# Performance work log

Measured on AMD Instinct MI355X. Metric: run time of the kernel, lower is better.

The kernel has to match this reference:

```python
import jax, jax.numpy as jnp
import numpy as np

B = 48        # graphs per batch
NODES = 330   # hardcoded in forward (x.view(batch_size, 330, hidden))
N = B * NODES # 15840 nodes
DEG = 16
E = N * DEG   # 253440 edges
IN_CH = 128
HID = 256
OUT_CH = 1
EDGE_DIM = 5
EPS = 1e-5


def _lin(key, out_f, in_f):
    k1, k2 = jax.random.split(key)
    s = 1.0 / np.sqrt(in_f)
    W = jax.random.uniform(k1, (out_f, in_f), minval=-s, maxval=s, dtype=jnp.float32)
    b = jax.random.uniform(k2, (out_f,), minval=-s, maxval=s, dtype=jnp.float32)
    return W, b


def setup_inputs() -> dict:
    key = jax.random.key(0)
    ks = jax.random.split(key, 10)
    x = jax.random.normal(ks[0], (N, IN_CH), dtype=jnp.float32)
    edge_index = jax.random.randint(ks[1], (2, E), 0, N, dtype=jnp.int32)
    edge_attr = jax.random.normal(ks[2], (E, EDGE_DIM), dtype=jnp.float32)
    batch = (jnp.arange(N, dtype=jnp.int32) // NODES)
    Wq, bq = _lin(ks[3], HID, IN_CH)
    Wk, bk = _lin(ks[4], HID, IN_CH)
    Wv, bv = _lin(ks[5], HID, IN_CH)
    se = 1.0 / np.sqrt(EDGE_DIM)
    We = jax.random.uniform(ks[6], (HID, EDGE_DIM), minval=-se, maxval=se, dtype=jnp.float32)  # lin_edge, bias=False
    Wskip, bskip = _lin(ks[7], HID, IN_CH)
    ln_g = jnp.ones((IN_CH,), jnp.float32); ln_b = jnp.zeros((IN_CH,), jnp.float32)
    bn_g = jnp.ones((HID,), jnp.float32); bn_b = jnp.zeros((HID,), jnp.float32)
    W1, b1 = _lin(ks[8], HID, HID)
    Wr, br = _lin(ks[9], OUT_CH, HID)
    return dict(x=x, edge_index=edge_index, edge_attr=edge_attr, batch=batch,
                Wq=Wq, bq=bq, Wk=Wk, bk=bk, Wv=Wv, bv=bv, We=We,
                Wskip=Wskip, bskip=bskip, ln_g=ln_g, ln_b=ln_b,
                bn_g=bn_g, bn_b=bn_b, W1=W1, b1=b1, Wr=Wr, br=br)


def _forward(x, edge_index, edge_attr, batch,
             Wq, bq, Wk, bk, Wv, bv, We, Wskip, bskip,
             ln_g, ln_b, bn_g, bn_b, W1, b1, Wr, br):
    n = x.shape[0]
    bs = batch.shape[0] // NODES
    # self.norm -> assumed LayerNorm over features
    mu = x.mean(-1, keepdims=True)
    var = x.var(-1, keepdims=True)
    x = (x - mu) / jnp.sqrt(var + EPS) * ln_g + ln_b

    # TransformerConv (heads=1, edge_dim=5, root_weight=True)
    src, dst = edge_index[0], edge_index[1]
    q = x @ Wq.T + bq                      # [N, HID]
    k = x @ Wk.T + bk
    v = x @ Wv.T + bv
    e = edge_attr @ We.T                   # [E, HID]
    ke = k[src] + e                        # edge-conditioned keys
    ve = v[src] + e                        # edge-conditioned values
    alpha = (q[dst] * ke).sum(-1) / jnp.sqrt(jnp.float32(HID))  # [E]
    m = jax.ops.segment_max(alpha, dst, num_segments=n)
    a = jnp.exp(alpha - m[dst])
    z = jax.ops.segment_sum(a, dst, num_segments=n)
    a = a / (z[dst] + 1e-16)               # PyG softmax guard
    out = jax.ops.segment_sum(a[:, None] * ve, dst, num_segments=n)
    out = out + x @ Wskip.T + bskip        # root/skip connection

    # BatchNorm1d (training-mode batch stats) + relu
    bm = out.mean(0)
    bv_ = out.var(0)
    out = (out - bm) / jnp.sqrt(bv_ + EPS) * bn_g + bn_b
    out = jax.nn.relu(out)

    # pooling chain over the node axis: 330 -> 110 -> 36 -> 18
    h = out.reshape(bs, NODES, HID).transpose(0, 2, 1)   # [B, HID, 330]
    h = h.reshape(bs, HID, 110, 3).max(-1)               # k3 s3
    h = h[:, :, :108].reshape(bs, HID, 36, 3).max(-1)    # k3 s3 (floor)
    h = h.reshape(bs, HID, 18, 2).max(-1)                # k2 s2
    h = h.transpose(0, 2, 1)                             # [B, 18, HID]

    h = jax.nn.relu(h @ W1.T + b1)
    c = (h @ Wr.T + br).mean(axis=1)                     # [B, OUT]
    return jax.nn.sigmoid(c).squeeze(-1)                 # [B]


def reference(x, edge_index, edge_attr, batch, Wq, bq, Wk, bk, Wv, bv, We,
              Wskip, bskip, ln_g, ln_b, bn_g, bn_b, W1, b1, Wr, br):
    return _forward(x, edge_index, edge_attr, batch, Wq, bq, Wk, bk, Wv, bv,
                    We, Wskip, bskip, ln_g, ln_b, bn_g, bn_b, W1, b1, Wr, br)
```

## Files before the change

kernel.cpp:

```cpp
#include <hip/hip_runtime.h>
#include <math.h>

#define NNODES 15840
#define NEDGES 253440
#define INCH 128
#define HIDC 256
#define BGR 48
#define GNODES 330
#define SLOT 56

typedef __attribute__((ext_vector_type(8))) short bf16x8;
typedef __attribute__((ext_vector_type(4))) float f32x4;
typedef __attribute__((ext_vector_type(2))) float f32x2;

__device__ inline unsigned short f2bf(float f) {
  union { float f; unsigned int u; } v; v.f = f;
  unsigned int u = v.u;
  u += 0x7fff + ((u >> 16) & 1);
  return (unsigned short)(u >> 16);
}
__device__ inline float bf2f(unsigned short h) {
  union { unsigned int u; float f; } v; v.u = ((unsigned int)h) << 16;
  return v.f;
}
__device__ inline unsigned char f2fp8(float f) {
  int p = __builtin_amdgcn_cvt_pk_fp8_f32(f, f, 0, false);
  return (unsigned char)(p & 0xff);
}

#define LN_BLOCKS 3960
#define WC_BLOCKS 128
#define BUILD_BLOCKS 990
__global__ __launch_bounds__(256) void prep_kernel(
    const float* __restrict__ x, const float* __restrict__ g, const float* __restrict__ b,
    unsigned short* __restrict__ Xhi, unsigned short* __restrict__ Xlo,
    const float* __restrict__ Wq, const float* __restrict__ bq,
    const float* __restrict__ Wk, const float* __restrict__ bk,
    const float* __restrict__ Wv, const float* __restrict__ bv,
    const float* __restrict__ Ws, const float* __restrict__ bs,
    unsigned short* __restrict__ Whi, unsigned short* __restrict__ Wlo,
    float* __restrict__ bbig,
    const int* __restrict__ src, const int* __restrict__ dst,
    const float* __restrict__ ea, int* __restrict__ cursor,
    int* __restrict__ src_perm, float* __restrict__ ea_perm) {
  int blk = blockIdx.x, t = threadIdx.x;
  if (blk < LN_BLOCKS) {
    int wid = blk * 4 + (t >> 6);
    int lane = t & 63;
    float2 v = *(const float2*)(x + (size_t)wid * INCH + lane * 2);
    float s = v.x + v.y;
#pragma unroll
    for (int o = 32; o > 0; o >>= 1) s += __shfl_xor(s, o);
    float mean = s * (1.0f / INCH);
    float d0 = v.x - mean, d1 = v.y - mean;
    float sq = d0 * d0 + d1 * d1;
#pragma unroll
    for (int o = 32; o > 0; o >>= 1) sq += __shfl_xor(sq, o);
    float rstd = rsqrtf(sq * (1.0f / INCH) + 1e-5f);
    float2 gg = *(const float2*)(g + lane * 2);
    float2 bb = *(const float2*)(b + lane * 2);
    float o0 = d0 * rstd * gg.x + bb.x;
    float o1 = d1 * rstd * gg.y + bb.y;
    unsigned short h0 = f2bf(o0), h1 = f2bf(o1);
    unsigned short l0 = f2bf(o0 - bf2f(h0)), l1 = f2bf(o1 - bf2f(h1));
    ushort2 hh; hh.x = h0; hh.y = h1;
    ushort2 ll; ll.x = l0; ll.y = l1;
    *(ushort2*)(Xhi + (size_t)wid * INCH + lane * 2) = hh;
    *(ushort2*)(Xlo + (size_t)wid * INCH + lane * 2) = ll;
  } else if (blk < LN_BLOCKS + WC_BLOCKS) {
    int idx = (blk - LN_BLOCKS) * 256 + t;
    int n = idx >> 5;
    int k0 = (idx & 31) * 4;
    const float* W;
    switch (n >> 8) {
      case 0:  W = Wq; break;
      case 1:  W = Wk; break;
      case 2:  W = Wv; break;
      default: W = Ws; break;
    }
    int r = n & 255;
    float4 w4 = *(const float4*)(W + (size_t)r * 128 + k0);
    ushort4 hi, lo;
    hi.x = f2bf(w4.x); lo.x = f2bf(w4.x - bf2f(hi.x));
    hi.y = f2bf(w4.y); lo.y = f2bf(w4.y - bf2f(hi.y));
    hi.z = f2bf(w4.z); lo.z = f2bf(w4.z - bf2f(hi.z));
    hi.w = f2bf(w4.w); lo.w = f2bf(w4.w - bf2f(hi.w));
    *(ushort4*)(Whi + (size_t)n * 128 + k0) = hi;
    *(ushort4*)(Wlo + (size_t)n * 128 + k0) = lo;
    if (idx < 1024) {
      const float* bsrc;
      switch (idx >> 8) {
        case 0:  bsrc = bq; break;
        case 1:  bsrc = bk; break;
        case 2:  bsrc = bv; break;
        default: bsrc = bs; break;
      }
      bbig[idx] = bsrc[idx & 255];
    }
  } else {
    int e = (blk - LN_BLOCKS - WC_BLOCKS) * 256 + t;
    if (e < NEDGES) {
      int d = dst[e];
      int pos = atomicAdd(&cursor[d], 1);
      if (pos < SLOT) {
        int slot = d * SLOT + pos;
        src_perm[slot] = src[e];
        const float* ap = ea + (size_t)e * 5;
        float* op = ea_perm + (size_t)slot * 5;
#pragma unroll
        for (int i = 0; i < 5; i++) op[i] = ap[i];
      }
    }
  }
}

__global__ __launch_bounds__(256, 2) void gemm_mfma(
    const unsigned short* __restrict__ Xhi, const unsigned short* __restrict__ Xlo,
    const unsigned short* __restrict__ Whi, const unsigned short* __restrict__ Wlo,
    const float* __restrict__ bbig,
    float* __restrict__ QS, unsigned char* __restrict__ KV8) {
  int lane = threadIdx.x & 63;
  int w = threadIdx.x >> 6;
  int m0 = blockIdx.x * 64;
  int quad = lane >> 4;
  int lr = lane & 15;

  const bf16x8 zf = {0, 0, 0, 0, 0, 0, 0, 0};
  bf16x8 A[4][2][4];
#pragma unroll
  for (int tI = 0; tI < 4; tI++) {
    int row = m0 + tI * 16 + lr;
    bool ok = row < NNODES;
    const unsigned short* ph = Xhi + (size_t)row * 128 + quad * 8;
    const unsigned short* pl = Xlo + (size_t)row * 128 + quad * 8;
#pragma unroll
    for (int kf = 0; kf < 4; kf++) {
      A[tI][0][kf] = ok ? *(const bf16x8*)(ph + kf * 32) : zf;
      A[tI][1][kf] = ok ? *(const bf16x8*)(pl + kf * 32) : zf;
    }
  }

  int ntbase = (blockIdx.y * 4 + w) * 8;
#pragma unroll 2
  for (int i = 0; i < 8; i++) {
    int n0 = (ntbase + i) * 16;
    const unsigned short* wh = Whi + (size_t)(n0 + lr) * 128 + quad * 8;
    const unsigned short* wl = Wlo + (size_t)(n0 + lr) * 128 + quad * 8;
    bf16x8 Bh[4], Bl[4];
#pragma unroll
    for (int kf = 0; kf < 4; kf++) {
      Bh[kf] = *(const bf16x8*)(wh + kf * 32);
      Bl[kf] = *(const bf16x8*)(wl + kf * 32);
    }
    f32x4 acc[4];
#pragma unroll
    for (int m = 0; m < 4; m++) acc[m] = (f32x4){0.f, 0.f, 0.f, 0.f};
#pragma unroll
    for (int kf = 0; kf < 4; kf++) {
#pragma unroll
      for (int m = 0; m < 4; m++)
        acc[m] = __builtin_amdgcn_mfma_f32_16x16x32_bf16(A[m][0][kf], Bh[kf], acc[m], 0, 0, 0);
#pragma unroll
      for (int m = 0; m < 4; m++)
        acc[m] = __builtin_amdgcn_mfma_f32_16x16x32_bf16(A[m][0][kf], Bl[kf], acc[m], 0, 0, 0);
#pragma unroll
      for (int m = 0; m < 4; m++)
        acc[m] = __builtin_amdgcn_mfma_f32_16x16x32_bf16(A[m][1][kf], Bh[kf], acc[m], 0, 0, 0);
    }
    int col = n0 + lr;
    float bias = bbig[col];
    int mat = col >> 8;
    int cc = col & 255;
    int base_off = (mat == 0 || mat == 1) ? cc : 256 + cc;
    bool isF32 = (mat == 0 || mat == 3);
#pragma unroll
    for (int m = 0; m < 4; m++) {
#pragma unroll
      for (int r = 0; r < 4; r++) {
        int row = m0 + m * 16 + quad * 4 + r;
        if (row < NNODES) {
          float val = acc[m][r] + bias;
          if (isF32) QS[(size_t)row * 512 + base_off] = val;
          else       KV8[(size_t)row * 512 + base_off] = f2fp8(val);
        }
      }
    }
  }
}

__global__ __launch_bounds__(256) void agg_kernel(
    const float* __restrict__ QS, const unsigned char* __restrict__ KV8,
    const float* __restrict__ ea_perm, const float* __restrict__ We,
    const int* __restrict__ src_perm, const int* __restrict__ cursor,
    float* __restrict__ outb) {
  int t = threadIdx.x;
  int nd = blockIdx.x * 4 + (t >> 6);
  int lane = t & 63;
  if (nd >= NNODES) return;

  float4 q = *(const float4*)(QS + (size_t)nd * 512 + 4 * lane);

  float c5[5];
  {
    float wp0[5], wp1[5], wp2[5], wp3[5];
#pragma unroll
    for (int d = 0; d < 5; d++) {
      wp0[d] = We[(4 * lane + 0) * 5 + d];
      wp1[d] = We[(4 * lane + 1) * 5 + d];
      wp2[d] = We[(4 * lane + 2) * 5 + d];
      wp3[d] = We[(4 * lane + 3) * 5 + d];
    }
#pragma unroll
    for (int d = 0; d < 5; d++) {
      float s = q.x * wp0[d] + q.y * wp1[d] + q.z * wp2[d] + q.w * wp3[d];
#pragma unroll
      for (int o = 32; o > 0; o >>= 1) s += __shfl_xor(s, o);
      c5[d] = s;
    }
  }

  int deg = cursor[nd]; if (deg > SLOT) deg = SLOT;
  int beg = nd * SLOT, end = beg + deg;
  float m = -INFINITY, z = 0.0f;
  float ax = 0.f, ay = 0.f, az = 0.f, aw = 0.f;
  float ea_acc[5] = {0.f, 0.f, 0.f, 0.f, 0.f};

  int j = beg;
  for (; j + 4 <= end; j += 4) {
    int s0 = src_perm[j], s1 = src_perm[j + 1], s2 = src_perm[j + 2], s3 = src_perm[j + 3];
    const unsigned char* b0 = KV8 + (size_t)s0 * 512 + 4 * lane;
    const unsigned char* b1 = KV8 + (size_t)s1 * 512 + 4 * lane;
    const unsigned char* b2 = KV8 + (size_t)s2 * 512 + 4 * lane;
    const unsigned char* b3 = KV8 + (size_t)s3 * 512 + 4 * lane;
    unsigned int kw0 = *(const unsigned int*)b0;
    unsigned int kw1 = *(const unsigned int*)b1;
    unsigned int kw2 = *(const unsigned int*)b2;
    unsigned int kw3 = *(const unsigned int*)b3;
    unsigned int vw0 = *(const unsigned int*)(b0 + 256);
    unsigned int vw1 = *(const unsigned int*)(b1 + 256);
    unsigned int vw2 = *(const unsigned int*)(b2 + 256);
    unsigned int vw3 = *(const unsigned int*)(b3 + 256);
    float eat[4][5];
    {
      const float* ap = ea_perm + (size_t)j * 5;
#pragma unroll
      for (int i = 0; i < 4; i++)
#pragma unroll
        for (int d = 0; d < 5; d++) eat[i][d] = ap[i * 5 + d];
    }
    f32x2 ka0 = __builtin_amdgcn_cvt_pk_f32_fp8(kw0, false), kb0 = __builtin_amdgcn_cvt_pk_f32_fp8(kw0, true);
    f32x2 ka1 = __builtin_amdgcn_cvt_pk_f32_fp8(kw1, false), kb1 = __builtin_amdgcn_cvt_pk_f32_fp8(kw1, true);
    f32x2 ka2 = __builtin_amdgcn_cvt_pk_f32_fp8(kw2, false), kb2 = __builtin_amdgcn_cvt_pk_f32_fp8(kw2, true);
    f32x2 ka3 = __builtin_amdgcn_cvt_pk_f32_fp8(kw3, false), kb3 = __builtin_amdgcn_cvt_pk_f32_fp8(kw3, true);
    float p0 = q.x * ka0.x + q.y * ka0.y + q.z * kb0.x + q.w * kb0.y;
    float p1 = q.x * ka1.x + q.y * ka1.y + q.z * kb1.x + q.w * kb1.y;
    float p2 = q.x * ka2.x + q.y * ka2.y + q.z * kb2.x + q.w * kb2.y;
    float p3 = q.x * ka3.x + q.y * ka3.y + q.z * kb3.x + q.w * kb3.y;
#pragma unroll
    for (int o = 32; o > 0; o >>= 1) {
      p0 += __shfl_xor(p0, o); p1 += __shfl_xor(p1, o);
      p2 += __shfl_xor(p2, o); p3 += __shfl_xor(p3, o);
    }
    float dt0 = 0.f, dt1 = 0.f, dt2 = 0.f, dt3 = 0.f;
#pragma unroll
    for (int d = 0; d < 5; d++) {
      dt0 += c5[d] * eat[0][d]; dt1 += c5[d] * eat[1][d];
      dt2 += c5[d] * eat[2][d]; dt3 += c5[d] * eat[3][d];
    }
    float al0 = (p0 + dt0) * 0.0625f, al1 = (p1 + dt1) * 0.0625f;
    float al2 = (p2 + dt2) * 0.0625f, al3 = (p3 + dt3) * 0.0625f;
    float bm = fmaxf(fmaxf(al0, al1), fmaxf(al2, al3));
    float nm = fmaxf(m, bm);
    float sc = __expf(m - nm);
    float w0 = __expf(al0 - nm), w1 = __expf(al1 - nm);
    float w2 = __expf(al2 - nm), w3 = __expf(al3 - nm);
    f32x2 va0 = __builtin_amdgcn_cvt_pk_f32_fp8(vw0, false), vb0 = __builtin_amdgcn_cvt_pk_f32_fp8(vw0, true);
    f32x2 va1 = __builtin_amdgcn_cvt_pk_f32_fp8(vw1, false), vb1 = __builtin_amdgcn_cvt_pk_f32_fp8(vw1, true);
    f32x2 va2 = __builtin_amdgcn_cvt_pk_f32_fp8(vw2, false), vb2 = __builtin_amdgcn_cvt_pk_f32_fp8(vw2, true);
    f32x2 va3 = __builtin_amdgcn_cvt_pk_f32_fp8(vw3, false), vb3 = __builtin_amdgcn_cvt_pk_f32_fp8(vw3, true);
    z = z * sc + (w0 + w1 + w2 + w3);
    ax = ax * sc + w0 * va0.x + w1 * va1.x + w2 * va2.x + w3 * va3.x;
    ay = ay * sc + w0 * va0.y + w1 * va1.y + w2 * va2.y + w3 * va3.y;
    az = az * sc + w0 * vb0.x + w1 * vb1.x + w2 * vb2.x + w3 * vb3.x;
    aw = aw * sc + w0 * vb0.y + w1 * vb1.y + w2 * vb2.y + w3 * vb3.y;
#pragma unroll
    for (int d = 0; d < 5; d++)
      ea_acc[d] = ea_acc[d] * sc + w0 * eat[0][d] + w1 * eat[1][d] + w2 * eat[2][d] + w3 * eat[3][d];
    m = nm;
  }
  for (; j < end; j++) {
    int s = src_perm[j];
    const unsigned char* bp = KV8 + (size_t)s * 512 + 4 * lane;
    unsigned int kw = *(const unsigned int*)bp;
    unsigned int vw = *(const unsigned int*)(bp + 256);
    float eat[5];
    const float* ap = ea_perm + (size_t)j * 5;
#pragma unroll
    for (int d = 0; d < 5; d++) eat[d] = ap[d];
    f32x2 ka = __builtin_amdgcn_cvt_pk_f32_fp8(kw, false), kb = __builtin_amdgcn_cvt_pk_f32_fp8(kw, true);
    float p = q.x * ka.x + q.y * ka.y + q.z * kb.x + q.w * kb.y;
#pragma unroll
    for (int o = 32; o > 0; o >>= 1) p += __shfl_xor(p, o);
    float dt = 0.f;
#pragma unroll
    for (int d = 0; d < 5; d++) dt += c5[d] * eat[d];
    float al = (p + dt) * 0.0625f;
    float nm = fmaxf(m, al);
    float sc = __expf(m - nm);
    float wgt = __expf(al - nm);
    f32x2 va = __builtin_amdgcn_cvt_pk_f32_fp8(vw, false), vb = __builtin_amdgcn_cvt_pk_f32_fp8(vw, true);
    z = z * sc + wgt;
    ax = ax * sc + wgt * va.x; ay = ay * sc + wgt * va.y;
    az = az * sc + wgt * vb.x; aw = aw * sc + wgt * vb.y;
#pragma unroll
    for (int d = 0; d < 5; d++) ea_acc[d] = ea_acc[d] * sc + wgt * eat[d];
    m = nm;
  }

  float inv = 1.0f / (z + 1e-16f);
  float4 sk = *(const float4*)(QS + (size_t)nd * 512 + 256 + 4 * lane);
  float efx = 0.f, efy = 0.f, efz = 0.f, efw = 0.f;
#pragma unroll
  for (int d = 0; d < 5; d++) {
    float ead = ea_acc[d];
    efx += We[(4 * lane + 0) * 5 + d] * ead;
    efy += We[(4 * lane + 1) * 5 + d] * ead;
    efz += We[(4 * lane + 2) * 5 + d] * ead;
    efw += We[(4 * lane + 3) * 5 + d] * ead;
  }
  float4 o;
  o.x = (ax + efx) * inv + sk.x;
  o.y = (ay + efy) * inv + sk.y;
  o.z = (az + efz) * inv + sk.z;
  o.w = (aw + efw) * inv + sk.w;
  *(float4*)(outb + (size_t)nd * HIDC + 4 * lane) = o;
}

__global__ void bnstat_kernel(const float* __restrict__ outb, float* __restrict__ sums,
                              float* __restrict__ sumsq) {
  int f = threadIdx.x;
  int r0 = blockIdx.x * 30;
  float s = 0.0f, sq = 0.0f;
  for (int r = 0; r < 30; r++) {
    float v = outb[(size_t)(r0 + r) * HIDC + f];
    s += v; sq += v * v;
  }
  atomicAdd(&sums[f], s);
  atomicAdd(&sumsq[f], sq);
}

__global__ __launch_bounds__(256) void pool_mlp_kernel(
    const float* __restrict__ outb, const float* __restrict__ sums,
    const float* __restrict__ sumsq, const float* __restrict__ bng,
    const float* __restrict__ bnb, const float* __restrict__ W1,
    const float* __restrict__ b1, const float* __restrict__ Wr,
    float* __restrict__ c) {
  __shared__ float hs[HIDC];
  __shared__ float red[HIDC];
  int bt = blockIdx.x, t = threadIdx.x;
  int b = bt / 18, tt = bt % 18;
  float mean = sums[t] * (1.0f / NNODES);
  float var = sumsq[t] * (1.0f / NNODES) - mean * mean;
  float scale = bng[t] * rsqrtf(var + 1e-5f);
  float shift = bnb[t] - mean * scale;
  int base = b * GNODES + tt * 18;
  float mx = -INFINITY;
  for (int r = 0; r < 18; r++) {
    float v = outb[(size_t)(base + r) * HIDC + t];
    mx = fmaxf(mx, fmaxf(v * scale + shift, 0.0f));
  }
  hs[t] = mx;
  __syncthreads();
  const float4* hv = (const float4*)hs;
  const float4* w = (const float4*)(W1 + t * HIDC);
  float acc = b1[t];
#pragma unroll 8
  for (int i = 0; i < HIDC / 4; i++) {
    float4 xi = hv[i]; float4 ww = w[i];
    acc += xi.x * ww.x + xi.y * ww.y + xi.z * ww.z + xi.w * ww.w;
  }
  red[t] = fmaxf(acc, 0.0f) * Wr[t];
  __syncthreads();
#pragma unroll
  for (int s = 128; s > 0; s >>= 1) {
    if (t < s) red[t] += red[t + s];
    __syncthreads();
  }
  if (t == 0) atomicAdd(&c[b], red[0] * (1.0f / 18.0f));
}

__global__ void final_kernel(const float* __restrict__ c, const float* __restrict__ br,
                             float* __restrict__ out) {
  int b = threadIdx.x;
  if (b < BGR) out[b] = 1.0f / (1.0f + expf(-(c[b] + br[0])));
}

extern "C" void kernel_launch(void* const* d_in, const int* in_sizes, int n_in,
                              void* d_out, int out_size, void* d_ws, size_t ws_size,
                              hipStream_t stream) {
  const float* x   = (const float*)d_in[0];
  const int*   ei  = (const int*)d_in[1];
  const float* ea  = (const float*)d_in[2];
  const float* Wq  = (const float*)d_in[4];  const float* bq  = (const float*)d_in[5];
  const float* Wk  = (const float*)d_in[6];  const float* bk  = (const float*)d_in[7];
  const float* Wv  = (const float*)d_in[8];  const float* bv  = (const float*)d_in[9];
  const float* We  = (const float*)d_in[10];
  const float* Wsk = (const float*)d_in[11]; const float* bsk = (const float*)d_in[12];
  const float* lng = (const float*)d_in[13]; const float* lnb = (const float*)d_in[14];
  const float* bng = (const float*)d_in[15]; const float* bnb = (const float*)d_in[16];
  const float* W1  = (const float*)d_in[17]; const float* b1  = (const float*)d_in[18];
  const float* Wr  = (const float*)d_in[19]; const float* br  = (const float*)d_in[20];
  float* outp = (float*)d_out;

  const int* srcArr = ei;
  const int* dstArr = ei + NEDGES;

  char* ws = (char*)d_ws;
  size_t off = 0;
  auto alloc = [&](size_t bytes) -> void* {
    void* p = ws + off;
    off += (bytes + 255) & ~(size_t)255;
    return p;
  };
  unsigned short* Xhi      = (unsigned short*)alloc((size_t)NNODES * INCH * 2);
  unsigned short* Xlo      = (unsigned short*)alloc((size_t)NNODES * INCH * 2);
  unsigned short* Whi      = (unsigned short*)alloc((size_t)1024 * 128 * 2);
  unsigned short* Wlo      = (unsigned short*)alloc((size_t)1024 * 128 * 2);
  float*          bbig     = (float*)alloc(1024 * 4);
  float*          QS       = (float*)alloc((size_t)NNODES * 512 * 4);
  unsigned char*  KV8      = (unsigned char*)alloc((size_t)NNODES * 512);
  float*          outb     = (float*)alloc((size_t)NNODES * HIDC * 4);
  int*            src_perm = (int*)alloc((size_t)NNODES * SLOT * 4);
  float*          ea_perm  = (float*)alloc((size_t)NNODES * SLOT * 5 * 4);
  size_t zn = (size_t)NNODES + HIDC * 2 + BGR;
  int* zblock = (int*)alloc(zn * 4);
  int*   cursor = zblock;
  float* sums   = (float*)(zblock + NNODES);
  float* sumsq  = sums + HIDC;
  float* cacc   = sumsq + HIDC;

  hipMemsetAsync(zblock, 0, zn * 4, stream);

  prep_kernel<<<LN_BLOCKS + WC_BLOCKS + BUILD_BLOCKS, 256, 0, stream>>>(
      x, lng, lnb, Xhi, Xlo, Wq, bq, Wk, bk, Wv, bv, Wsk, bsk, Whi, Wlo, bbig,
      srcArr, dstArr, ea, cursor, src_perm, ea_perm);
  gemm_mfma<<<dim3(248, 2), 256, 0, stream>>>(Xhi, Xlo, Whi, Wlo, bbig, QS, KV8);
  agg_kernel<<<NNODES / 4, 256, 0, stream>>>(QS, KV8, ea_perm, We, src_perm, cursor, outb);
  bnstat_kernel<<<528, 256, 0, stream>>>(outb, sums, sumsq);
  pool_mlp_kernel<<<BGR * 18, 256, 0, stream>>>(outb, sums, sumsq, bng, bnb, W1, b1, Wr, cacc);
  final_kernel<<<1, 64, 0, stream>>>(cacc, br, outp);
}
```

Measured before the change: 253.5 us.

## Pack edge src and attributes into 32-byte records and unroll aggregation by 8

The separate src_perm and ea_perm arrays are merged into one 8-float record per edge slot (source index bit-cast plus 5 attributes, padded), written with two float4 stores. The aggregation loop now processes 8 edges per iteration with two vector loads per edge and one clamped, masked tail in place of a separate scalar remainder loop. This is meant to cut load instruction count and raise memory-level parallelism for the gathered K/V reads. In exchange the padded layout moves more bytes, and masked tail lanes do redundant gathers for nodes whose degree is not a multiple of 8.

After: 282.9 us. 11.6% more time.

```diff
diff --git a/kernel.cpp b/kernel.cpp
--- a/kernel.cpp
+++ b/kernel.cpp
@@ -42,7 +42,7 @@
     float* __restrict__ bbig,
     const int* __restrict__ src, const int* __restrict__ dst,
     const float* __restrict__ ea, int* __restrict__ cursor,
-    int* __restrict__ src_perm, float* __restrict__ ea_perm) {
+    float* __restrict__ pack) {
   int blk = blockIdx.x, t = threadIdx.x;
   if (blk < LN_BLOCKS) {
     int wid = blk * 4 + (t >> 6);
@@ -103,12 +103,14 @@
       int d = dst[e];
       int pos = atomicAdd(&cursor[d], 1);
       if (pos < SLOT) {
-        int slot = d * SLOT + pos;
-        src_perm[slot] = src[e];
+        float* op = pack + ((size_t)d * SLOT + pos) * 8;
         const float* ap = ea + (size_t)e * 5;
-        float* op = ea_perm + (size_t)slot * 5;
-#pragma unroll
-        for (int i = 0; i < 5; i++) op[i] = ap[i];
+        float4 r0, r1;
+        r0.x = __int_as_float(src[e]);
+        r0.y = ap[0]; r0.z = ap[1]; r0.w = ap[2];
+        r1.x = ap[3]; r1.y = ap[4]; r1.z = 0.f; r1.w = 0.f;
+        *(float4*)op = r0;
+        *(float4*)(op + 4) = r1;
       }
     }
   }
@@ -190,9 +192,8 @@
 
 __global__ __launch_bounds__(256) void agg_kernel(
     const float* __restrict__ QS, const unsigned char* __restrict__ KV8,
-    const float* __restrict__ ea_perm, const float* __restrict__ We,
-    const int* __restrict__ src_perm, const int* __restrict__ cursor,
-    float* __restrict__ outb) {
+    const float* __restrict__ pack, const float* __restrict__ We,
+    const int* __restrict__ cursor, float* __restrict__ outb) {
   int t = threadIdx.x;
   int nd = blockIdx.x * 4 + (t >> 6);
   int lane = t & 63;
@@ -225,95 +226,68 @@
   float ax = 0.f, ay = 0.f, az = 0.f, aw = 0.f;
   float ea_acc[5] = {0.f, 0.f, 0.f, 0.f, 0.f};
 
-  int j = beg;
-  for (; j + 4 <= end; j += 4) {
-    int s0 = src_perm[j], s1 = src_perm[j + 1], s2 = src_perm[j + 2], s3 = src_perm[j + 3];
-    const unsigned char* b0 = KV8 + (size_t)s0 * 512 + 4 * lane;
-    const unsigned char* b1 = KV8 + (size_t)s1 * 512 + 4 * lane;
-    const unsigned char* b2 = KV8 + (size_t)s2 * 512 + 4 * lane;
-    const unsigned char* b3 = KV8 + (size_t)s3 * 512 + 4 * lane;
-    unsigned int kw0 = *(const unsigned int*)b0;
-    unsigned int kw1 = *(const unsigned int*)b1;
-    unsigned int kw2 = *(const unsigned int*)b2;
-    unsigned int kw3 = *(const unsigned int*)b3;
-    unsigned int vw0 = *(const unsigned int*)(b0 + 256);
-    unsigned int vw1 = *(const unsigned int*)(b1 + 256);
-    unsigned int vw2 = *(const unsigned int*)(b2 + 256);
-    unsigned int vw3 = *(const unsigned int*)(b3 + 256);
-    float eat[4][5];
-    {
-      const float* ap = ea_perm + (size_t)j * 5;
-#pragma unroll
-      for (int i = 0; i < 4; i++)
-#pragma unroll
-        for (int d = 0; d < 5; d++) eat[i][d] = ap[i * 5 + d];
-    }
-    f32x2 ka0 = __builtin_amdgcn_cvt_pk_f32_fp8(kw0, false), kb0 = __builtin_amdgcn_cvt_pk_f32_fp8(kw0, true);
-    f32x2 ka1 = __builtin_amdgcn_cvt_pk_f32_fp8(kw1, false), kb1 = __builtin_amdgcn_cvt_pk_f32_fp8(kw1, true);
-    f32x2 ka2 = __builtin_amdgcn_cvt_pk_f32_fp8(kw2, false), kb2 = __builtin_amdgcn_cvt_pk_f32_fp8(kw2, true);
-    f32x2 ka3 = __builtin_amdgcn_cvt_pk_f32_fp8(kw3, false), kb3 = __builtin_amdgcn_cvt_pk_f32_fp8(kw3, true);
-    float p0 = q.x * ka0.x + q.y * ka0.y + q.z * kb0.x + q.w * kb0.y;
-    float p1 = q.x * ka1.x + q.y * ka1.y + q.z * kb1.x + q.w * kb1.y;
-    float p2 = q.x * ka2.x + q.y * ka2.y + q.z * kb2.x + q.w * kb2.y;
-    float p3 = q.x * ka3.x + q.y * ka3.y + q.z * kb3.x + q.w * kb3.y;
+  for (int j0 = beg; j0 < end; j0 += 8) {
+    float4 pr0[8], pr1[8];
+#pragma unroll
+    for (int i = 0; i < 8; i++) {
+      int jj = j0 + i; jj = (jj < end) ? jj : (end - 1);
+      const float4* pp = (const float4*)(pack + (size_t)jj * 8);
+      pr0[i] = pp[0];
+      pr1[i] = pp[1];
+    }
+    unsigned int kw[8], vw[8];
+#pragma unroll
+    for (int i = 0; i < 8; i++) {
+      int s = __float_as_int(pr0[i].x);
+      const unsigned char* bp = KV8 + (size_t)s * 512 + 4 * lane;
+      kw[i] = *(const unsigned int*)bp;
+      vw[i] = *(const unsigned int*)(bp + 256);
+    }
+    float p[8];
+#pragma unroll
+    for (int i = 0; i < 8; i++) {
+      f32x2 ka = __builtin_amdgcn_cvt_pk_f32_fp8(kw[i], false);
+      f32x2 kb = __builtin_amdgcn_cvt_pk_f32_fp8(kw[i], true);
+      p[i] = q.x * ka.x + q.y * ka.y + q.z * kb.x + q.w * kb.y;
+    }
 #pragma unroll
     for (int o = 32; o > 0; o >>= 1) {
-      p0 += __shfl_xor(p0, o); p1 += __shfl_xor(p1, o);
-      p2 += __shfl_xor(p2, o); p3 += __shfl_xor(p3, o);
-    }
-    float dt0 = 0.f, dt1 = 0.f, dt2 = 0.f, dt3 = 0.f;
-#pragma unroll
-    for (int d = 0; d < 5; d++) {
-      dt0 += c5[d] * eat[0][d]; dt1 += c5[d] * eat[1][d];
-      dt2 += c5[d] * eat[2][d]; dt3 += c5[d] * eat[3][d];
-    }
-    float al0 = (p0 + dt0) * 0.0625f, al1 = (p1 + dt1) * 0.0625f;
-    float al2 = (p2 + dt2) * 0.0625f, al3 = (p3 + dt3) * 0.0625f;
-    float bm = fmaxf(fmaxf(al0, al1), fmaxf(al2, al3));
+#pragma unroll
+      for (int i = 0; i < 8; i++) p[i] += __shfl_xor(p[i], o);
+    }
+    float al[8];
+    float bm = -1e30f;
+#pragma unroll
+    for (int i = 0; i < 8; i++) {
+      float dt = c5[0] * pr0[i].y + c5[1] * pr0[i].z + c5[2] * pr0[i].w +
+                 c5[3] * pr1[i].x + c5[4] * pr1[i].y;
+      float a = (p[i] + dt) * 0.0625f;
+      al[i] = (j0 + i < end) ? a : -1e30f;
+      bm = fmaxf(bm, al[i]);
+    }
     float nm = fmaxf(m, bm);
     float sc = __expf(m - nm);
-    float w0 = __expf(al0 - nm), w1 = __expf(al1 - nm);
-    float w2 = __expf(al2 - nm), w3 = __expf(al3 - nm);
-    f32x2 va0 = __builtin_amdgcn_cvt_pk_f32_fp8(vw0, false), vb0 = __builtin_amdgcn_cvt_pk_f32_fp8(vw0, true);
-    f32x2 va1 = __builtin_amdgcn_cvt_pk_f32_fp8(vw1, false), vb1 = __builtin_amdgcn_cvt_pk_f32_fp8(vw1, true);
-    f32x2 va2 = __builtin_amdgcn_cvt_pk_f32_fp8(vw2, false), vb2 = __builtin_amdgcn_cvt_pk_f32_fp8(vw2, true);
-    f32x2 va3 = __builtin_amdgcn_cvt_pk_f32_fp8(vw3, false), vb3 = __builtin_amdgcn_cvt_pk_f32_fp8(vw3, true);
-    z = z * sc + (w0 + w1 + w2 + w3);
-    ax = ax * sc + w0 * va0.x + w1 * va1.x + w2 * va2.x + w3 * va3.x;
-    ay = ay * sc + w0 * va0.y + w1 * va1.y + w2 * va2.y + w3 * va3.y;
-    az = az * sc + w0 * vb0.x + w1 * vb1.x + w2 * vb2.x + w3 * vb3.x;
-    aw = aw * sc + w0 * vb0.y + w1 * vb1.y + w2 * vb2.y + w3 * vb3.y;
-#pragma unroll
-    for (int d = 0; d < 5; d++)
-      ea_acc[d] = ea_acc[d] * sc + w0 * eat[0][d] + w1 * eat[1][d] + w2 * eat[2][d] + w3 * eat[3][d];
-    m = nm;
-  }
-  for (; j < end; j++) {
-    int s = src_perm[j];
-    const unsigned char* bp = KV8 + (size_t)s * 512 + 4 * lane;
-    unsigned int kw = *(const unsigned int*)bp;
-    unsigned int vw = *(const unsigned int*)(bp + 256);
-    float eat[5];
-    const float* ap = ea_perm + (size_t)j * 5;
-#pragma unroll
-    for (int d = 0; d < 5; d++) eat[d] = ap[d];
-    f32x2 ka = __builtin_amdgcn_cvt_pk_f32_fp8(kw, false), kb = __builtin_amdgcn_cvt_pk_f32_fp8(kw, true);
-    float p = q.x * ka.x + q.y * ka.y + q.z * kb.x + q.w * kb.y;
-#pragma unroll
-    for (int o = 32; o > 0; o >>= 1) p += __shfl_xor(p, o);
-    float dt = 0.f;
-#pragma unroll
-    for (int d = 0; d < 5; d++) dt += c5[d] * eat[d];
-    float al = (p + dt) * 0.0625f;
-    float nm = fmaxf(m, al);
-    float sc = __expf(m - nm);
-    float wgt = __expf(al - nm);
-    f32x2 va = __builtin_amdgcn_cvt_pk_f32_fp8(vw, false), vb = __builtin_amdgcn_cvt_pk_f32_fp8(vw, true);
-    z = z * sc + wgt;
-    ax = ax * sc + wgt * va.x; ay = ay * sc + wgt * va.y;
-    az = az * sc + wgt * vb.x; aw = aw * sc + wgt * vb.y;
-#pragma unroll
-    for (int d = 0; d < 5; d++) ea_acc[d] = ea_acc[d] * sc + wgt * eat[d];
+    float wg[8];
+#pragma unroll
+    for (int i = 0; i < 8; i++) wg[i] = __expf(al[i] - nm);
+    float zs = 0.f, sx = 0.f, sy = 0.f, sz2 = 0.f, sw = 0.f;
+    float se[5] = {0.f, 0.f, 0.f, 0.f, 0.f};
+#pragma unroll
+    for (int i = 0; i < 8; i++) {
+      f32x2 va = __builtin_amdgcn_cvt_pk_f32_fp8(vw[i], false);
+      f32x2 vb = __builtin_amdgcn_cvt_pk_f32_fp8(vw[i], true);
+      zs += wg[i];
+      sx += wg[i] * va.x; sy += wg[i] * va.y;
+      sz2 += wg[i] * vb.x; sw += wg[i] * vb.y;
+      se[0] += wg[i] * pr0[i].y; se[1] += wg[i] * pr0[i].z;
+      se[2] += wg[i] * pr0[i].w; se[3] += wg[i] * pr1[i].x;
+      se[4] += wg[i] * pr1[i].y;
+    }
+    z = z * sc + zs;
+    ax = ax * sc + sx; ay = ay * sc + sy;
+    az = az * sc + sz2; aw = aw * sc + sw;
+#pragma unroll
+    for (int d = 0; d < 5; d++) ea_acc[d] = ea_acc[d] * sc + se[d];
     m = nm;
   }
 
@@ -430,8 +404,7 @@
   float*          QS       = (float*)alloc((size_t)NNODES * 512 * 4);
   unsigned char*  KV8      = (unsigned char*)alloc((size_t)NNODES * 512);
   float*          outb     = (float*)alloc((size_t)NNODES * HIDC * 4);
-  int*            src_perm = (int*)alloc((size_t)NNODES * SLOT * 4);
-  float*          ea_perm  = (float*)alloc((size_t)NNODES * SLOT * 5 * 4);
+  float*          pack     = (float*)alloc((size_t)NNODES * SLOT * 32);
   size_t zn = (size_t)NNODES + HIDC * 2 + BGR;
   int* zblock = (int*)alloc(zn * 4);
   int*   cursor = zblock;
@@ -443,9 +416,9 @@
 
   prep_kernel<<<LN_BLOCKS + WC_BLOCKS + BUILD_BLOCKS, 256, 0, stream>>>(
       x, lng, lnb, Xhi, Xlo, Wq, bq, Wk, bk, Wv, bv, Wsk, bsk, Whi, Wlo, bbig,
-      srcArr, dstArr, ea, cursor, src_perm, ea_perm);
+      srcArr, dstArr, ea, cursor, pack);
   gemm_mfma<<<dim3(248, 2), 256, 0, stream>>>(Xhi, Xlo, Whi, Wlo, bbig, QS, KV8);
-  agg_kernel<<<NNODES / 4, 256, 0, stream>>>(QS, KV8, ea_perm, We, src_perm, cursor, outb);
+  agg_kernel<<<NNODES / 4, 256, 0, stream>>>(QS, KV8, pack, We, cursor, outb);
   bnstat_kernel<<<528, 256, 0, stream>>>(outb, sums, sumsq);
   pool_mlp_kernel<<<BGR * 18, 256, 0, stream>>>(outb, sums, sumsq, bng, bnb, W1, b1, Wr, cacc);
   final_kernel<<<1, 64, 0, stream>>>(cacc, br, outp);
```

## Fuse BN statistics into aggregation and sigmoid into pooling kernel

Applied to the files above, without the earlier changes.

Computes per-feature batchnorm sums and sums of squares inside the aggregation kernel: each block reduces its four nodes through shared memory and then adds atomically. This removes the separate stats kernel and its reread of the output buffer. The final sigmoid moves into the pool/MLP kernel through a last-block-done counter, removing another launch. In exchange, many more global atomics hit the same 512 addresses.

After: 331.8 us. +30.9%, slower.

```diff
diff --git a/kernel.cpp b/kernel.cpp
--- a/kernel.cpp
+++ b/kernel.cpp
@@ -192,11 +192,12 @@
     const float* __restrict__ QS, const unsigned char* __restrict__ KV8,
     const float* __restrict__ ea_perm, const float* __restrict__ We,
     const int* __restrict__ src_perm, const int* __restrict__ cursor,
-    float* __restrict__ outb) {
+    float* __restrict__ outb, float* __restrict__ sums, float* __restrict__ sumsq) {
+  __shared__ float4 plv[4][64];
   int t = threadIdx.x;
-  int nd = blockIdx.x * 4 + (t >> 6);
+  int w = t >> 6;
+  int nd = blockIdx.x * 4 + w;
   int lane = t & 63;
-  if (nd >= NNODES) return;
 
   float4 q = *(const float4*)(QS + (size_t)nd * 512 + 4 * lane);
 
@@ -334,19 +335,18 @@
   o.z = (az + efz) * inv + sk.z;
   o.w = (aw + efw) * inv + sk.w;
   *(float4*)(outb + (size_t)nd * HIDC + 4 * lane) = o;
-}
-
-__global__ void bnstat_kernel(const float* __restrict__ outb, float* __restrict__ sums,
-                              float* __restrict__ sumsq) {
-  int f = threadIdx.x;
-  int r0 = blockIdx.x * 30;
-  float s = 0.0f, sq = 0.0f;
-  for (int r = 0; r < 30; r++) {
-    float v = outb[(size_t)(r0 + r) * HIDC + f];
+
+  plv[w][lane] = o;
+  __syncthreads();
+  float s = 0.f, sq = 0.f;
+#pragma unroll
+  for (int ww = 0; ww < 4; ww++) {
+    const float* pp = (const float*)&plv[ww][t >> 2];
+    float v = pp[t & 3];
     s += v; sq += v * v;
   }
-  atomicAdd(&sums[f], s);
-  atomicAdd(&sumsq[f], sq);
+  atomicAdd(&sums[t], s);
+  atomicAdd(&sumsq[t], sq);
 }
 
 __global__ __launch_bounds__(256) void pool_mlp_kernel(
@@ -354,7 +354,8 @@
     const float* __restrict__ sumsq, const float* __restrict__ bng,
     const float* __restrict__ bnb, const float* __restrict__ W1,
     const float* __restrict__ b1, const float* __restrict__ Wr,
-    float* __restrict__ c) {
+    const float* __restrict__ br, float* __restrict__ cacc,
+    int* __restrict__ done, float* __restrict__ out) {
   __shared__ float hs[HIDC];
   __shared__ float red[HIDC];
   int bt = blockIdx.x, t = threadIdx.x;
@@ -386,13 +387,18 @@
     if (t < s) red[t] += red[t + s];
     __syncthreads();
   }
-  if (t == 0) atomicAdd(&c[b], red[0] * (1.0f / 18.0f));
-}
-
-__global__ void final_kernel(const float* __restrict__ c, const float* __restrict__ br,
-                             float* __restrict__ out) {
-  int b = threadIdx.x;
-  if (b < BGR) out[b] = 1.0f / (1.0f + expf(-(c[b] + br[0])));
+  if (t == 0) {
+    atomicAdd(&cacc[b], red[0] * (1.0f / 18.0f));
+    __threadfence();
+    int old = atomicAdd(done, 1);
+    if (old == BGR * 18 - 1) {
+      float brv = br[0];
+      for (int g = 0; g < BGR; g++) {
+        float cv = atomicAdd(&cacc[g], 0.0f);
+        out[g] = 1.0f / (1.0f + expf(-(cv + brv)));
+      }
+    }
+  }
 }
 
 extern "C" void kernel_launch(void* const* d_in, const int* in_sizes, int n_in,
@@ -432,12 +438,13 @@
   float*          outb     = (float*)alloc((size_t)NNODES * HIDC * 4);
   int*            src_perm = (int*)alloc((size_t)NNODES * SLOT * 4);
   float*          ea_perm  = (float*)alloc((size_t)NNODES * SLOT * 5 * 4);
-  size_t zn = (size_t)NNODES + HIDC * 2 + BGR;
+  size_t zn = (size_t)NNODES + HIDC * 2 + BGR + 1;
   int* zblock = (int*)alloc(zn * 4);
   int*   cursor = zblock;
   float* sums   = (float*)(zblock + NNODES);
   float* sumsq  = sums + HIDC;
   float* cacc   = sumsq + HIDC;
+  int*   done   = (int*)(cacc + BGR);
 
   hipMemsetAsync(zblock, 0, zn * 4, stream);
 
@@ -445,8 +452,8 @@
       x, lng, lnb, Xhi, Xlo, Wq, bq, Wk, bk, Wv, bv, Wsk, bsk, Whi, Wlo, bbig,
       srcArr, dstArr, ea, cursor, src_perm, ea_perm);
   gemm_mfma<<<dim3(248, 2), 256, 0, stream>>>(Xhi, Xlo, Whi, Wlo, bbig, QS, KV8);
-  agg_kernel<<<NNODES / 4, 256, 0, stream>>>(QS, KV8, ea_perm, We, src_perm, cursor, outb);
-  bnstat_kernel<<<528, 256, 0, stream>>>(outb, sums, sumsq);
-  pool_mlp_kernel<<<BGR * 18, 256, 0, stream>>>(outb, sums, sumsq, bng, bnb, W1, b1, Wr, cacc);
-  final_kernel<<<1, 64, 0, stream>>>(cacc, br, outp);
-}
+  agg_kernel<<<NNODES / 4, 256, 0, stream>>>(QS, KV8, ea_perm, We, src_perm, cursor,
+                                             outb, sums, sumsq);
+  pool_mlp_kernel<<<BGR * 18, 256, 0, stream>>>(outb, sums, sumsq, bng, bnb, W1, b1, Wr,
+                                                br, cacc, done, outp);
+}
```
